# Kernel optimization log

Measured on AMD Instinct MI355X. Metric: run time of the kernel, lower is better.

The kernel has to match this reference:

```python
import jax, jax.numpy as jnp
import numpy as np

B, S, N, E = 8, 32, 2000, 64000
GH, H = 32, 64  # gat_h, lstm hidden
NEG_SLOPE = 0.2


def setup_inputs() -> dict:
    key = jax.random.key(0)
    ks = jax.random.split(key, 12)
    f32 = jnp.float32
    x = jax.random.normal(ks[0], (B, S, N), f32)
    edge_index = jax.random.randint(ks[1], (2, E), 0, N)
    # GATConv(1, GH, heads=1, concat=False): lin weight [GH,1] -> vector, att_src/att_dst [GH], bias [GH]
    w_lin = jax.random.normal(ks[2], (GH,), f32)
    att_src = jax.random.normal(ks[3], (GH,), f32) * 0.1
    att_dst = jax.random.normal(ks[4], (GH,), f32) * 0.1
    gat_bias = jax.random.normal(ks[5], (GH,), f32) * 0.01
    D = GH * N  # LSTM input size
    W_ih = jax.random.normal(ks[6], (4 * H, D), f32) * (1.0 / np.sqrt(D))
    W_hh = jax.random.normal(ks[7], (4 * H, H), f32) * (1.0 / np.sqrt(H))
    b_ih = jax.random.normal(ks[8], (4 * H,), f32) * 0.01
    b_hh = jax.random.normal(ks[9], (4 * H,), f32) * 0.01
    W_head = jax.random.normal(ks[10], (N, H), f32) * (1.0 / np.sqrt(H))
    b_head = jax.random.normal(ks[11], (N,), f32) * 0.01
    return {"x": x, "edge_index": edge_index, "w_lin": w_lin, "att_src": att_src,
            "att_dst": att_dst, "gat_bias": gat_bias, "W_ih": W_ih, "W_hh": W_hh,
            "b_ih": b_ih, "b_hh": b_hh, "W_head": W_head, "b_head": b_head}


def reference(x, edge_index, w_lin, att_src, att_dst, gat_bias,
              W_ih, W_hh, b_ih, b_hh, W_head, b_head):
    x = x.astype(jnp.float32)
    # --- GAT (in_channels=1, heads=1), batched over (B,S) ---
    # PyG default: add self-loops
    loops = jnp.arange(N)
    ei = jnp.concatenate([edge_index, jnp.stack([loops, loops])], axis=1)
    src, dst = ei[0], ei[1]  # [Et], Et = E + N
    # lifted feature h_n = x_n * w_lin (rank-1), so attention logits are scalar per node
    a_src = x * jnp.dot(w_lin, att_src)  # [B,S,N]
    a_dst = x * jnp.dot(w_lin, att_dst)  # [B,S,N]
    e = jax.nn.leaky_relu(a_src[..., src] + a_dst[..., dst], NEG_SLOPE)  # [B,S,Et]
    e = jnp.moveaxis(e, -1, 0)  # [Et,B,S] (segment axis leading)
    seg_max = jax.ops.segment_max(e, dst, num_segments=N)  # [N,B,S]
    e = jnp.exp(e - seg_max[dst])
    denom = jax.ops.segment_sum(e, dst, num_segments=N)  # [N,B,S]
    alpha = e / denom[dst]  # edge softmax over incoming edges
    x_src = jnp.moveaxis(x[..., src], -1, 0)  # [Et,B,S]
    agg = jax.ops.segment_sum(alpha * x_src, dst, num_segments=N)  # [N,B,S]
    agg = jnp.moveaxis(agg, 0, -1)  # [B,S,N]
    # outer product with w_lin restores [.,GH]; add bias, then relu (from forward)
    h = jax.nn.relu(agg[..., None] * w_lin + gat_bias)  # [B,S,N,GH]
    lstm_in = h.reshape(B, S, N * GH)

    # --- LSTM (1 layer, batch_first), keep final hidden state ---
    def step(carry, xt):
        hp, cp = carry
        gates = xt @ W_ih.T + b_ih + hp @ W_hh.T + b_hh  # [B,4H]
        i, f, g, o = jnp.split(gates, 4, axis=-1)
        c = jax.nn.sigmoid(f) * cp + jax.nn.sigmoid(i) * jnp.tanh(g)
        hn = jax.nn.sigmoid(o) * jnp.tanh(c)
        return (hn, c), None

    h0 = jnp.zeros((B, H), jnp.float32)
    c0 = jnp.zeros((B, H), jnp.float32)
    (hT, _), _ = jax.lax.scan(step, (h0, c0), jnp.swapaxes(lstm_in, 0, 1))
    return hT @ W_head.T + b_head  # [B,N]
```

## Files before the change

### kernel.cpp

```cpp
#include <hip/hip_runtime.h>
#include <hip/hip_bf16.h>
#include <cstddef>
#include <cstdint>

#define B_  8
#define S_  32
#define BT_ 256
#define N_  2000
#define E_  64000
#define GH_ 32
#define H_  64
#define G4_ 256
#define D_  64000
#define NEG_SLOPE_ 0.2f

#define KC_   125
#define NPC_  16

typedef __attribute__((ext_vector_type(8))) short short8;
typedef __attribute__((ext_vector_type(4))) float floatx4;
union U8 { uint32_t u[4]; short8 s; };

__device__ __forceinline__ float fsigmoid(float x) { return 1.0f / (1.0f + __expf(-x)); }
__device__ __forceinline__ float ftanh_(float x)   { return 1.0f - 2.0f / (__expf(2.0f * x) + 1.0f); }

__device__ __forceinline__ void split2(float v0, float v1, uint32_t& hi, uint32_t& lo) {
  uint32_t b0 = __float_as_uint(v0), b1 = __float_as_uint(v1);
  uint32_t h0 = b0 & 0xffff0000u,    h1 = b1 & 0xffff0000u;
  hi = (b0 >> 16) | h1;
  float l0 = v0 - __uint_as_float(h0);
  float l1 = v1 - __uint_as_float(h1);
  lo = (__float_as_uint(l0) >> 16) | (__float_as_uint(l1) & 0xffff0000u);
}


__global__ __launch_bounds__(256) void hist_kernel(
    const int* __restrict__ ei, int* __restrict__ deg)
{
  const int i = blockIdx.x * 256 + threadIdx.x;
  if (i < E_) atomicAdd(&deg[ei[E_ + i]], 1);
}

__global__ __launch_bounds__(256) void scan_kernel(
    const int* __restrict__ deg, int* __restrict__ rowptr, int* __restrict__ cursor)
{
  __shared__ int tsum[256];
  const int tid = threadIdx.x;
  int v[8];
  int s = 0;
  const int base = tid * 8;
#pragma unroll
  for (int j = 0; j < 8; ++j) {
    const int idx = base + j;
    const int d = (idx < N_) ? deg[idx] : 0;
    v[j] = s;
    s += d;
  }
  tsum[tid] = s;
  __syncthreads();
  for (int off = 1; off < 256; off <<= 1) {
    int t = 0;
    if (tid >= off) t = tsum[tid - off];
    __syncthreads();
    tsum[tid] += t;
    __syncthreads();
  }
  const int ebase = tsum[tid] - s;
#pragma unroll
  for (int j = 0; j < 8; ++j) {
    const int idx = base + j;
    if (idx < N_) {
      const int r = ebase + v[j];
      rowptr[idx] = r;
      cursor[idx] = r;
    }
  }
  if (tid == 0) rowptr[N_] = E_;
}

__global__ __launch_bounds__(256) void scatter_kernel(
    const int* __restrict__ ei, int* __restrict__ cursor, int* __restrict__ csr_src)
{
  const int i = blockIdx.x * 256 + threadIdx.x;
  if (i >= E_) return;
  const int s = ei[i];
  const int d = ei[E_ + i];
  const int pos = atomicAdd(&cursor[d], 1);
  csr_src[pos] = s;
}

__global__ __launch_bounds__(256) void transpose_kernel(
    const float* __restrict__ x, float* __restrict__ xT)
{
  __shared__ float tile[32][33];
  const int tx = threadIdx.x & 31;
  const int ty = threadIdx.x >> 5;
  const int n0  = blockIdx.x * 32;
  const int bt0 = blockIdx.y * 32;
#pragma unroll
  for (int r = 0; r < 4; ++r) {
    const int bt = bt0 + ty + r * 8;
    const int nn = n0 + tx;
    if (nn < N_) tile[ty + r * 8][tx] = x[(size_t)bt * N_ + nn];
  }
  __syncthreads();
#pragma unroll
  for (int r = 0; r < 4; ++r) {
    const int n = n0 + ty + r * 8;
    if (n < N_) xT[(size_t)n * BT_ + bt0 + tx] = tile[tx][ty + r * 8];
  }
}

__global__ __launch_bounds__(256) void gat_gather_kernel(
    const float* __restrict__ xT, const int* __restrict__ rowptr,
    const int* __restrict__ csr_src,
    const float* __restrict__ w_lin, const float* __restrict__ att_src,
    const float* __restrict__ att_dst, float* __restrict__ agg_T)
{
  __shared__ int srcs[512];
  const int n   = blockIdx.x;
  const int tid = threadIdx.x;

  float c_s = 0.f, c_d = 0.f;
  for (int g = 0; g < GH_; ++g) {
    const float w = w_lin[g];
    c_s += w * att_src[g];
    c_d += w * att_dst[g];
  }

  const int r0 = rowptr[n];
  const int r1 = rowptr[n + 1];
  const int d  = r1 - r0;
  for (int i = tid; i < d && i < 512; i += 256) srcs[i] = csr_src[r0 + i];
  __syncthreads();

  const float xn = xT[(size_t)n * BT_ + tid];
  float e = (c_s + c_d) * xn;
  e = e > 0.f ? e : NEG_SLOPE_ * e;
  float w = __expf(e);
  float num = w * xn;
  float den = w;

  for (int p = 0; p < d; ++p) {
    int s;
    if (p < 512) s = srcs[p]; else s = csr_src[r0 + p];
    const float xs = xT[(size_t)s * BT_ + tid];
    float ee = c_s * xs + c_d * xn;
    ee = ee > 0.f ? ee : NEG_SLOPE_ * ee;
    const float ww = __expf(ee);
    num += ww * xs;
    den += ww;
  }
  agg_T[(size_t)n * BT_ + tid] = num / den;
}

__global__ __launch_bounds__(256) void gate_mfma_kernel(
    const float* __restrict__ W_ih, const float* __restrict__ agg_T,
    const float* __restrict__ w_lin, const float* __restrict__ gat_bias,
    float* __restrict__ partial, float* __restrict__ pre_gates, int use_atomic)
{
  __shared__ float agg_s[NPC_ * 256];

  const int tid  = threadIdx.x;
  const int nb   = blockIdx.x;
  const int kc   = blockIdx.y;
  const int n0   = kc * NPC_;
  const int wv   = tid >> 6;
  const int lane = tid & 63;
  const int i16  = lane & 15;
  const int q    = lane >> 4;
  const int jw   = nb * 64 + wv * 16;

  {
    const float4* src = (const float4*)(agg_T + (size_t)n0 * 256);
    float4* dst = (float4*)agg_s;
#pragma unroll
    for (int p = 0; p < 4; ++p) dst[tid + p * 256] = src[tid + p * 256];
  }

  float wlr[8], gbr[8];
#pragma unroll
  for (int j = 0; j < 8; ++j) {
    wlr[j] = w_lin[q * 8 + j];
    gbr[j] = gat_bias[q * 8 + j];
  }

  floatx4 acc[16];
#pragma unroll
  for (int mt = 0; mt < 16; ++mt)
#pragma unroll
    for (int r = 0; r < 4; ++r) acc[mt][r] = 0.f;

  __syncthreads();

  const float* Wrow = W_ih + (size_t)(jw + i16) * D_ + (size_t)n0 * GH_ + q * 8;

  float4 cb0 = *(const float4*)(Wrow);
  float4 cb1 = *(const float4*)(Wrow + 4);

#pragma unroll 1
  for (int nn = 0; nn < NPC_; ++nn) {
    const int nnx = (nn + 1) & (NPC_ - 1);
    float4 pb0 = *(const float4*)(Wrow + nnx * GH_);
    float4 pb1 = *(const float4*)(Wrow + nnx * GH_ + 4);

    short8 bh, bl;
    {
      U8 Hh, Ll;
      split2(cb0.x, cb0.y, Hh.u[0], Ll.u[0]);
      split2(cb0.z, cb0.w, Hh.u[1], Ll.u[1]);
      split2(cb1.x, cb1.y, Hh.u[2], Ll.u[2]);
      split2(cb1.z, cb1.w, Hh.u[3], Ll.u[3]);
      bh = Hh.s; bl = Ll.s;
    }

#pragma unroll
    for (int mt = 0; mt < 16; ++mt) {
      const float a = agg_s[nn * 256 + mt * 16 + i16];
      U8 Ah, Al;
#pragma unroll
      for (int p = 0; p < 4; ++p) {
        float v0 = fmaf(a, wlr[2 * p],     gbr[2 * p]);
        float v1 = fmaf(a, wlr[2 * p + 1], gbr[2 * p + 1]);
        v0 = fmaxf(v0, 0.f);
        v1 = fmaxf(v1, 0.f);
        split2(v0, v1, Ah.u[p], Al.u[p]);
      }
      acc[mt] = __builtin_amdgcn_mfma_f32_16x16x32_bf16(Ah.s, bh, acc[mt], 0, 0, 0);
      acc[mt] = __builtin_amdgcn_mfma_f32_16x16x32_bf16(Al.s, bh, acc[mt], 0, 0, 0);
      acc[mt] = __builtin_amdgcn_mfma_f32_16x16x32_bf16(Ah.s, bl, acc[mt], 0, 0, 0);
    }
    cb0 = pb0; cb1 = pb1;
  }

  const int j = jw + i16;
#pragma unroll
  for (int mt = 0; mt < 16; ++mt) {
    const int bt = mt * 16 + q * 4;
    if (use_atomic) {
#pragma unroll
      for (int r = 0; r < 4; ++r) atomicAdd(&pre_gates[(bt + r) * G4_ + j], acc[mt][r]);
    } else {
#pragma unroll
      for (int r = 0; r < 4; ++r)
        partial[((size_t)kc * 256 + (bt + r)) * 256 + j] = acc[mt][r];
    }
  }
}

__global__ __launch_bounds__(256) void reduce_kernel(
    const float* __restrict__ partial, float* __restrict__ pre_gates)
{
  const int o = blockIdx.x * 256 + threadIdx.x;
  float s0 = 0.f, s1 = 0.f, s2 = 0.f, s3 = 0.f;
  int kc = 0;
  for (; kc + 4 <= KC_; kc += 4) {
    s0 += partial[(size_t)(kc + 0) * 65536 + o];
    s1 += partial[(size_t)(kc + 1) * 65536 + o];
    s2 += partial[(size_t)(kc + 2) * 65536 + o];
    s3 += partial[(size_t)(kc + 3) * 65536 + o];
  }
  for (; kc < KC_; ++kc) s0 += partial[(size_t)kc * 65536 + o];
  pre_gates[o] = (s0 + s1) + (s2 + s3);
}

__global__ __launch_bounds__(256) void lstm_kernel(
    const float* __restrict__ pre_gates, const float* __restrict__ W_hh,
    const float* __restrict__ b_ih, const float* __restrict__ b_hh,
    float* __restrict__ hT)
{
  const int b   = blockIdx.x;
  const int tid = threadIdx.x;
  __shared__ float h_s[H_];
  __shared__ float g_s[G4_];

  float wr[H_];
#pragma unroll
  for (int k = 0; k < H_; ++k) wr[k] = W_hh[(size_t)tid * H_ + k];

  float pg[S_];
#pragma unroll
  for (int t = 0; t < S_; ++t) pg[t] = pre_gates[(size_t)(b * S_ + t) * G4_ + tid];

  const float bias = b_ih[tid] + b_hh[tid];
  if (tid < H_) h_s[tid] = 0.f;
  float c = 0.f;
  __syncthreads();

  for (int t = 0; t < S_; ++t) {
    float g0 = pg[t] + bias, g1 = 0.f, g2 = 0.f, g3 = 0.f;
#pragma unroll
    for (int k = 0; k < H_; k += 4) {
      g0 = fmaf(wr[k + 0], h_s[k + 0], g0);
      g1 = fmaf(wr[k + 1], h_s[k + 1], g1);
      g2 = fmaf(wr[k + 2], h_s[k + 2], g2);
      g3 = fmaf(wr[k + 3], h_s[k + 3], g3);
    }
    g_s[tid] = (g0 + g1) + (g2 + g3);
    __syncthreads();
    if (tid < H_) {
      const float ig = fsigmoid(g_s[tid]);
      const float fg = fsigmoid(g_s[H_ + tid]);
      const float gg = ftanh_(g_s[2 * H_ + tid]);
      const float og = fsigmoid(g_s[3 * H_ + tid]);
      c = fg * c + ig * gg;
      h_s[tid] = og * ftanh_(c);
    }
    __syncthreads();
  }
  if (tid < H_) hT[b * H_ + tid] = h_s[tid];
}

__global__ __launch_bounds__(256) void head_kernel(
    const float* __restrict__ hT, const float* __restrict__ W_head,
    const float* __restrict__ b_head, float* __restrict__ out)
{
  const int o = blockIdx.x * 256 + threadIdx.x;
  if (o >= B_ * N_) return;
  const int b = o / N_;
  const int n = o - b * N_;
  const float4* w4 = (const float4*)(W_head + (size_t)n * H_);
  const float4* h4 = (const float4*)(hT + (size_t)b * H_);
  float acc = b_head[n];
#pragma unroll
  for (int q = 0; q < H_ / 4; ++q) {
    const float4 w = w4[q];
    const float4 h = h4[q];
    acc += w.x * h.x + w.y * h.y + w.z * h.z + w.w * h.w;
  }
  out[o] = acc;
}

extern "C" void kernel_launch(void* const* d_in, const int* in_sizes, int n_in,
                              void* d_out, int out_size, void* d_ws, size_t ws_size,
                              hipStream_t stream) {
  const float* x        = (const float*)d_in[0];
  const int*   ei       = (const int*)  d_in[1];
  const float* w_lin    = (const float*)d_in[2];
  const float* att_src  = (const float*)d_in[3];
  const float* att_dst  = (const float*)d_in[4];
  const float* gat_bias = (const float*)d_in[5];
  const float* W_ih     = (const float*)d_in[6];
  const float* W_hh     = (const float*)d_in[7];
  const float* b_ih     = (const float*)d_in[8];
  const float* b_hh     = (const float*)d_in[9];
  const float* W_head   = (const float*)d_in[10];
  const float* b_head   = (const float*)d_in[11];
  float* out = (float*)d_out;

  char* ws = (char*)d_ws;
  float* agg_T     = (float*)(ws + 0);
  float* pre_gates = (float*)(ws + 2048000);
  float* hT        = (float*)(ws + 2310144);
  float* xT        = (float*)(ws + 2312192);
  int*   deg       = (int*)  (ws + 4360192);
  int*   rowptr    = (int*)  (ws + 4368384);
  int*   cursor    = (int*)  (ws + 4376576);
  int*   csr_src   = (int*)  (ws + 4384768);
  float* partial   = (float*)(ws + 4640768);
  const size_t need = 4640768 + (size_t)KC_ * 65536 * sizeof(float);
  const int use_atomic = (ws_size < need) ? 1 : 0;

  hipMemsetAsync(deg, 0, N_ * sizeof(int), stream);
  hist_kernel<<<dim3((E_ + 255) / 256), dim3(256), 0, stream>>>(ei, deg);
  scan_kernel<<<dim3(1), dim3(256), 0, stream>>>(deg, rowptr, cursor);
  scatter_kernel<<<dim3((E_ + 255) / 256), dim3(256), 0, stream>>>(ei, cursor, csr_src);
  transpose_kernel<<<dim3((N_ + 31) / 32, BT_ / 32), dim3(256), 0, stream>>>(x, xT);
  gat_gather_kernel<<<dim3(N_), dim3(256), 0, stream>>>(
      xT, rowptr, csr_src, w_lin, att_src, att_dst, agg_T);

  if (use_atomic) {
    hipMemsetAsync(pre_gates, 0, G4_ * BT_ * sizeof(float), stream);
  }
  gate_mfma_kernel<<<dim3(4, KC_), dim3(256), 0, stream>>>(
      W_ih, agg_T, w_lin, gat_bias, partial, pre_gates, use_atomic);
  if (!use_atomic) {
    reduce_kernel<<<dim3(256), dim3(256), 0, stream>>>(partial, pre_gates);
  }

  lstm_kernel<<<dim3(B_), dim3(256), 0, stream>>>(pre_gates, W_hh, b_ih, b_hh, hT);
  head_kernel<<<dim3((B_ * N_ + 255) / 256), dim3(256), 0, stream>>>(hT, W_head, b_head, out);
}
```

Measured before the change: 249.4 us.

## Materialize fp16 GAT features and switch gate GEMM to single fp16 MFMA

The GAT gather kernel now expands each aggregated value through w_lin, bias and ReLU and writes a 32-wide fp16 feature tensor (about 32 MB). The gate GEMM reads this directly and uses one fp16 MFMA per tile instead of three bf16 split-precision MFMAs, with a new tiling of 8x50 blocks, 40 nodes per chunk and fewer partials to reduce. CSR construction is merged into a single-block kernel using shared-memory atomics, and the head projection is fused into the LSTM kernel. This drops precision to plain fp16 and adds a large extra memory write and read in exchange for fewer MFMAs and fewer launches.

```diff
diff --git a/kernel.cpp b/kernel.cpp
--- a/kernel.cpp
+++ b/kernel.cpp
@@ -14,79 +14,54 @@
 #define D_  64000
 #define NEG_SLOPE_ 0.2f
 
-#define KC_   125
-#define NPC_  16
-
-typedef __attribute__((ext_vector_type(8))) short short8;
+#define KC2_  50
+#define NPC2_ 40
+
+typedef __attribute__((ext_vector_type(8))) _Float16 half8;
 typedef __attribute__((ext_vector_type(4))) float floatx4;
-union U8 { uint32_t u[4]; short8 s; };
 
 __device__ __forceinline__ float fsigmoid(float x) { return 1.0f / (1.0f + __expf(-x)); }
 __device__ __forceinline__ float ftanh_(float x)   { return 1.0f - 2.0f / (__expf(2.0f * x) + 1.0f); }
 
-__device__ __forceinline__ void split2(float v0, float v1, uint32_t& hi, uint32_t& lo) {
-  uint32_t b0 = __float_as_uint(v0), b1 = __float_as_uint(v1);
-  uint32_t h0 = b0 & 0xffff0000u,    h1 = b1 & 0xffff0000u;
-  hi = (b0 >> 16) | h1;
-  float l0 = v0 - __uint_as_float(h0);
-  float l1 = v1 - __uint_as_float(h1);
-  lo = (__float_as_uint(l0) >> 16) | (__float_as_uint(l1) & 0xffff0000u);
-}
-
-
-__global__ __launch_bounds__(256) void hist_kernel(
-    const int* __restrict__ ei, int* __restrict__ deg)
-{
-  const int i = blockIdx.x * 256 + threadIdx.x;
-  if (i < E_) atomicAdd(&deg[ei[E_ + i]], 1);
-}
-
-__global__ __launch_bounds__(256) void scan_kernel(
-    const int* __restrict__ deg, int* __restrict__ rowptr, int* __restrict__ cursor)
-{
-  __shared__ int tsum[256];
+__global__ __launch_bounds__(1024) void csr_build_kernel(
+    const int* __restrict__ ei, int* __restrict__ rowptr, int* __restrict__ csr_src)
+{
+  __shared__ int deg_s[N_];
+  __shared__ int cur_s[N_];
+  __shared__ int tsum[1024];
   const int tid = threadIdx.x;
-  int v[8];
-  int s = 0;
-  const int base = tid * 8;
-#pragma unroll
-  for (int j = 0; j < 8; ++j) {
-    const int idx = base + j;
-    const int d = (idx < N_) ? deg[idx] : 0;
-    v[j] = s;
-    s += d;
-  }
-  tsum[tid] = s;
-  __syncthreads();
-  for (int off = 1; off < 256; off <<= 1) {
+
+  for (int n = tid; n < N_; n += 1024) deg_s[n] = 0;
+  __syncthreads();
+
+  for (int i = tid; i < E_; i += 1024) atomicAdd(&deg_s[ei[E_ + i]], 1);
+  __syncthreads();
+
+  const int i0 = tid * 2, i1 = tid * 2 + 1;
+  const int d0 = (i0 < N_) ? deg_s[i0] : 0;
+  const int d1 = (i1 < N_) ? deg_s[i1] : 0;
+  const int sl = d0 + d1;
+  tsum[tid] = sl;
+  __syncthreads();
+  for (int off = 1; off < 1024; off <<= 1) {
     int t = 0;
     if (tid >= off) t = tsum[tid - off];
     __syncthreads();
     tsum[tid] += t;
     __syncthreads();
   }
-  const int ebase = tsum[tid] - s;
-#pragma unroll
-  for (int j = 0; j < 8; ++j) {
-    const int idx = base + j;
-    if (idx < N_) {
-      const int r = ebase + v[j];
-      rowptr[idx] = r;
-      cursor[idx] = r;
-    }
-  }
+  const int ebase = tsum[tid] - sl;
+  if (i0 < N_) { rowptr[i0] = ebase;      cur_s[i0] = ebase; }
+  if (i1 < N_) { rowptr[i1] = ebase + d0; cur_s[i1] = ebase + d0; }
   if (tid == 0) rowptr[N_] = E_;
-}
-
-__global__ __launch_bounds__(256) void scatter_kernel(
-    const int* __restrict__ ei, int* __restrict__ cursor, int* __restrict__ csr_src)
-{
-  const int i = blockIdx.x * 256 + threadIdx.x;
-  if (i >= E_) return;
-  const int s = ei[i];
-  const int d = ei[E_ + i];
-  const int pos = atomicAdd(&cursor[d], 1);
-  csr_src[pos] = s;
+  __syncthreads();
+
+  for (int i = tid; i < E_; i += 1024) {
+    const int s = ei[i];
+    const int d = ei[E_ + i];
+    const int pos = atomicAdd(&cur_s[d], 1);
+    csr_src[pos] = s;
+  }
 }
 
 __global__ __launch_bounds__(256) void transpose_kernel(
@@ -111,13 +86,15 @@
   }
 }
 
-__global__ __launch_bounds__(256) void gat_gather_kernel(
+__global__ __launch_bounds__(256) void gat_gather_expand_kernel(
     const float* __restrict__ xT, const int* __restrict__ rowptr,
     const int* __restrict__ csr_src,
     const float* __restrict__ w_lin, const float* __restrict__ att_src,
-    const float* __restrict__ att_dst, float* __restrict__ agg_T)
+    const float* __restrict__ att_dst, const float* __restrict__ gat_bias,
+    _Float16* __restrict__ A)
 {
   __shared__ int srcs[512];
+  __shared__ float wl_s[GH_], gb_s[GH_];
   const int n   = blockIdx.x;
   const int tid = threadIdx.x;
 
@@ -127,6 +104,7 @@
     c_s += w * att_src[g];
     c_d += w * att_dst[g];
   }
+  if (tid < GH_) { wl_s[tid] = w_lin[tid]; gb_s[tid] = gat_bias[tid]; }
 
   const int r0 = rowptr[n];
   const int r1 = rowptr[n + 1];
@@ -151,99 +129,105 @@
     num += ww * xs;
     den += ww;
   }
-  agg_T[(size_t)n * BT_ + tid] = num / den;
-}
-
-__global__ __launch_bounds__(256) void gate_mfma_kernel(
-    const float* __restrict__ W_ih, const float* __restrict__ agg_T,
-    const float* __restrict__ w_lin, const float* __restrict__ gat_bias,
+  const float aggv = num / den;
+
+  half8 buf[4];
+#pragma unroll
+  for (int q = 0; q < 4; ++q)
+#pragma unroll
+    for (int j = 0; j < 8; ++j) {
+      const int g = q * 8 + j;
+      float v = fmaf(aggv, wl_s[g], gb_s[g]);
+      v = fmaxf(v, 0.f);
+      buf[q][j] = (_Float16)v;
+    }
+  half8* dst = (half8*)(A + ((size_t)n * BT_ + tid) * GH_);
+#pragma unroll
+  for (int q = 0; q < 4; ++q) dst[q] = buf[q];
+}
+
+__global__ __launch_bounds__(256) void gate_mfma2_kernel(
+    const float* __restrict__ W_ih, const _Float16* __restrict__ A,
     float* __restrict__ partial, float* __restrict__ pre_gates, int use_atomic)
 {
-  __shared__ float agg_s[NPC_ * 256];
-
   const int tid  = threadIdx.x;
   const int nb   = blockIdx.x;
   const int kc   = blockIdx.y;
-  const int n0   = kc * NPC_;
+  const int n0   = kc * NPC2_;
   const int wv   = tid >> 6;
   const int lane = tid & 63;
   const int i16  = lane & 15;
   const int q    = lane >> 4;
-  const int jw   = nb * 64 + wv * 16;
-
-  {
-    const float4* src = (const float4*)(agg_T + (size_t)n0 * 256);
-    float4* dst = (float4*)agg_s;
-#pragma unroll
-    for (int p = 0; p < 4; ++p) dst[tid + p * 256] = src[tid + p * 256];
-  }
-
-  float wlr[8], gbr[8];
-#pragma unroll
-  for (int j = 0; j < 8; ++j) {
-    wlr[j] = w_lin[q * 8 + j];
-    gbr[j] = gat_bias[q * 8 + j];
-  }
-
-  floatx4 acc[16];
-#pragma unroll
-  for (int mt = 0; mt < 16; ++mt)
-#pragma unroll
-    for (int r = 0; r < 4; ++r) acc[mt][r] = 0.f;
-
-  __syncthreads();
-
-  const float* Wrow = W_ih + (size_t)(jw + i16) * D_ + (size_t)n0 * GH_ + q * 8;
-
-  float4 cb0 = *(const float4*)(Wrow);
-  float4 cb1 = *(const float4*)(Wrow + 4);
+  const int jn0  = nb * 32;
+
+  floatx4 acc[4][2];
+#pragma unroll
+  for (int mt = 0; mt < 4; ++mt)
+#pragma unroll
+    for (int nt = 0; nt < 2; ++nt)
+#pragma unroll
+      for (int r = 0; r < 4; ++r) acc[mt][nt][r] = 0.f;
+
+  const _Float16* Ap = A + ((size_t)n0 * BT_ + wv * 64 + i16) * GH_ + q * 8;
+
+  const float* Bp0 = W_ih + (size_t)(jn0 + i16) * D_ + (size_t)n0 * GH_ + q * 8;
+  const float* Bp1 = Bp0 + (size_t)16 * D_;
+
+  float4 b0a = *(const float4*)(Bp0);
+  float4 b0b = *(const float4*)(Bp0 + 4);
+  float4 b1a = *(const float4*)(Bp1);
+  float4 b1b = *(const float4*)(Bp1 + 4);
 
 #pragma unroll 1
-  for (int nn = 0; nn < NPC_; ++nn) {
-    const int nnx = (nn + 1) & (NPC_ - 1);
-    float4 pb0 = *(const float4*)(Wrow + nnx * GH_);
-    float4 pb1 = *(const float4*)(Wrow + nnx * GH_ + 4);
-
-    short8 bh, bl;
-    {
-      U8 Hh, Ll;
-      split2(cb0.x, cb0.y, Hh.u[0], Ll.u[0]);
-      split2(cb0.z, cb0.w, Hh.u[1], Ll.u[1]);
-      split2(cb1.x, cb1.y, Hh.u[2], Ll.u[2]);
-      split2(cb1.z, cb1.w, Hh.u[3], Ll.u[3]);
-      bh = Hh.s; bl = Ll.s;
-    }
-
-#pragma unroll
-    for (int mt = 0; mt < 16; ++mt) {
-      const float a = agg_s[nn * 256 + mt * 16 + i16];
-      U8 Ah, Al;
-#pragma unroll
-      for (int p = 0; p < 4; ++p) {
-        float v0 = fmaf(a, wlr[2 * p],     gbr[2 * p]);
-        float v1 = fmaf(a, wlr[2 * p + 1], gbr[2 * p + 1]);
-        v0 = fmaxf(v0, 0.f);
-        v1 = fmaxf(v1, 0.f);
-        split2(v0, v1, Ah.u[p], Al.u[p]);
+  for (int nn = 0; nn < NPC2_; ++nn) {
+    half8 a0 = *(const half8*)(Ap + 0 * 512);
+    half8 a1 = *(const half8*)(Ap + 1 * 512);
+    half8 a2 = *(const half8*)(Ap + 2 * 512);
+    half8 a3 = *(const half8*)(Ap + 3 * 512);
+
+    const int nx = (nn + 1 < NPC2_) ? (nn + 1) : nn;
+    float4 p0a = *(const float4*)(Bp0 + nx * GH_);
+    float4 p0b = *(const float4*)(Bp0 + nx * GH_ + 4);
+    float4 p1a = *(const float4*)(Bp1 + nx * GH_);
+    float4 p1b = *(const float4*)(Bp1 + nx * GH_ + 4);
+
+    half8 bf0, bf1;
+    bf0[0] = (_Float16)b0a.x; bf0[1] = (_Float16)b0a.y;
+    bf0[2] = (_Float16)b0a.z; bf0[3] = (_Float16)b0a.w;
+    bf0[4] = (_Float16)b0b.x; bf0[5] = (_Float16)b0b.y;
+    bf0[6] = (_Float16)b0b.z; bf0[7] = (_Float16)b0b.w;
+    bf1[0] = (_Float16)b1a.x; bf1[1] = (_Float16)b1a.y;
+    bf1[2] = (_Float16)b1a.z; bf1[3] = (_Float16)b1a.w;
+    bf1[4] = (_Float16)b1b.x; bf1[5] = (_Float16)b1b.y;
+    bf1[6] = (_Float16)b1b.z; bf1[7] = (_Float16)b1b.w;
+
+    acc[0][0] = __builtin_amdgcn_mfma_f32_16x16x32_f16(a0, bf0, acc[0][0], 0, 0, 0);
+    acc[1][0] = __builtin_amdgcn_mfma_f32_16x16x32_f16(a1, bf0, acc[1][0], 0, 0, 0);
+    acc[2][0] = __builtin_amdgcn_mfma_f32_16x16x32_f16(a2, bf0, acc[2][0], 0, 0, 0);
+    acc[3][0] = __builtin_amdgcn_mfma_f32_16x16x32_f16(a3, bf0, acc[3][0], 0, 0, 0);
+    acc[0][1] = __builtin_amdgcn_mfma_f32_16x16x32_f16(a0, bf1, acc[0][1], 0, 0, 0);
+    acc[1][1] = __builtin_amdgcn_mfma_f32_16x16x32_f16(a1, bf1, acc[1][1], 0, 0, 0);
+    acc[2][1] = __builtin_amdgcn_mfma_f32_16x16x32_f16(a2, bf1, acc[2][1], 0, 0, 0);
+    acc[3][1] = __builtin_amdgcn_mfma_f32_16x16x32_f16(a3, bf1, acc[3][1], 0, 0, 0);
+
+    b0a = p0a; b0b = p0b; b1a = p1a; b1b = p1b;
+    Ap += (size_t)BT_ * GH_;
+  }
+
+#pragma unroll
+  for (int mt = 0; mt < 4; ++mt) {
+    const int bt = wv * 64 + mt * 16 + q * 4;
+#pragma unroll
+    for (int nt = 0; nt < 2; ++nt) {
+      const int j = jn0 + nt * 16 + i16;
+      if (use_atomic) {
+#pragma unroll
+        for (int r = 0; r < 4; ++r) atomicAdd(&pre_gates[(bt + r) * G4_ + j], acc[mt][nt][r]);
+      } else {
+#pragma unroll
+        for (int r = 0; r < 4; ++r)
+          partial[((size_t)kc * BT_ + (bt + r)) * G4_ + j] = acc[mt][nt][r];
       }
-      acc[mt] = __builtin_amdgcn_mfma_f32_16x16x32_bf16(Ah.s, bh, acc[mt], 0, 0, 0);
-      acc[mt] = __builtin_amdgcn_mfma_f32_16x16x32_bf16(Al.s, bh, acc[mt], 0, 0, 0);
-      acc[mt] = __builtin_amdgcn_mfma_f32_16x16x32_bf16(Ah.s, bl, acc[mt], 0, 0, 0);
-    }
-    cb0 = pb0; cb1 = pb1;
-  }
-
-  const int j = jw + i16;
-#pragma unroll
-  for (int mt = 0; mt < 16; ++mt) {
-    const int bt = mt * 16 + q * 4;
-    if (use_atomic) {
-#pragma unroll
-      for (int r = 0; r < 4; ++r) atomicAdd(&pre_gates[(bt + r) * G4_ + j], acc[mt][r]);
-    } else {
-#pragma unroll
-      for (int r = 0; r < 4; ++r)
-        partial[((size_t)kc * 256 + (bt + r)) * 256 + j] = acc[mt][r];
     }
   }
 }
@@ -252,22 +236,21 @@
     const float* __restrict__ partial, float* __restrict__ pre_gates)
 {
   const int o = blockIdx.x * 256 + threadIdx.x;
-  float s0 = 0.f, s1 = 0.f, s2 = 0.f, s3 = 0.f;
+  float s0 = 0.f, s1 = 0.f;
   int kc = 0;
-  for (; kc + 4 <= KC_; kc += 4) {
+  for (; kc + 2 <= KC2_; kc += 2) {
     s0 += partial[(size_t)(kc + 0) * 65536 + o];
     s1 += partial[(size_t)(kc + 1) * 65536 + o];
-    s2 += partial[(size_t)(kc + 2) * 65536 + o];
-    s3 += partial[(size_t)(kc + 3) * 65536 + o];
-  }
-  for (; kc < KC_; ++kc) s0 += partial[(size_t)kc * 65536 + o];
-  pre_gates[o] = (s0 + s1) + (s2 + s3);
-}
-
-__global__ __launch_bounds__(256) void lstm_kernel(
+  }
+  for (; kc < KC2_; ++kc) s0 += partial[(size_t)kc * 65536 + o];
+  pre_gates[o] = s0 + s1;
+}
+
+__global__ __launch_bounds__(256) void lstm_head_kernel(
     const float* __restrict__ pre_gates, const float* __restrict__ W_hh,
     const float* __restrict__ b_ih, const float* __restrict__ b_hh,
-    float* __restrict__ hT)
+    const float* __restrict__ W_head, const float* __restrict__ b_head,
+    float* __restrict__ out)
 {
   const int b   = blockIdx.x;
   const int tid = threadIdx.x;
@@ -308,27 +291,18 @@
     }
     __syncthreads();
   }
-  if (tid < H_) hT[b * H_ + tid] = h_s[tid];
-}
-
-__global__ __launch_bounds__(256) void head_kernel(
-    const float* __restrict__ hT, const float* __restrict__ W_head,
-    const float* __restrict__ b_head, float* __restrict__ out)
-{
-  const int o = blockIdx.x * 256 + threadIdx.x;
-  if (o >= B_ * N_) return;
-  const int b = o / N_;
-  const int n = o - b * N_;
-  const float4* w4 = (const float4*)(W_head + (size_t)n * H_);
-  const float4* h4 = (const float4*)(hT + (size_t)b * H_);
-  float acc = b_head[n];
-#pragma unroll
-  for (int q = 0; q < H_ / 4; ++q) {
-    const float4 w = w4[q];
-    const float4 h = h4[q];
-    acc += w.x * h.x + w.y * h.y + w.z * h.z + w.w * h.w;
-  }
-  out[o] = acc;
+
+  for (int n = tid; n < N_; n += 256) {
+    const float4* w4 = (const float4*)(W_head + (size_t)n * H_);
+    float acc = b_head[n];
+#pragma unroll
+    for (int qq = 0; qq < H_ / 4; ++qq) {
+      const float4 w = w4[qq];
+      acc += w.x * h_s[qq * 4 + 0] + w.y * h_s[qq * 4 + 1] +
+             w.z * h_s[qq * 4 + 2] + w.w * h_s[qq * 4 + 3];
+    }
+    out[(size_t)b * N_ + n] = acc;
+  }
 }
 
 extern "C" void kernel_launch(void* const* d_in, const int* in_sizes, int n_in,
@@ -349,35 +323,29 @@
   float* out = (float*)d_out;
 
   char* ws = (char*)d_ws;
-  float* agg_T     = (float*)(ws + 0);
-  float* pre_gates = (float*)(ws + 2048000);
-  float* hT        = (float*)(ws + 2310144);
-  float* xT        = (float*)(ws + 2312192);
-  int*   deg       = (int*)  (ws + 4360192);
-  int*   rowptr    = (int*)  (ws + 4368384);
-  int*   cursor    = (int*)  (ws + 4376576);
-  int*   csr_src   = (int*)  (ws + 4384768);
-  float* partial   = (float*)(ws + 4640768);
-  const size_t need = 4640768 + (size_t)KC_ * 65536 * sizeof(float);
+  float*     xT        = (float*)    (ws + 0);
+  _Float16*  A         = (_Float16*) (ws + 2048000);
+  float*     pre_gates = (float*)    (ws + 34816000);
+  int*       rowptr    = (int*)      (ws + 35078144);
+  int*       csr_src   = (int*)      (ws + 35086336);
+  float*     partial   = (float*)    (ws + 35342336);
+  const size_t need = 35342336 + (size_t)KC2_ * 65536 * sizeof(float);
   const int use_atomic = (ws_size < need) ? 1 : 0;
 
-  hipMemsetAsync(deg, 0, N_ * sizeof(int), stream);
-  hist_kernel<<<dim3((E_ + 255) / 256), dim3(256), 0, stream>>>(ei, deg);
-  scan_kernel<<<dim3(1), dim3(256), 0, stream>>>(deg, rowptr, cursor);
-  scatter_kernel<<<dim3((E_ + 255) / 256), dim3(256), 0, stream>>>(ei, cursor, csr_src);
+  csr_build_kernel<<<dim3(1), dim3(1024), 0, stream>>>(ei, rowptr, csr_src);
   transpose_kernel<<<dim3((N_ + 31) / 32, BT_ / 32), dim3(256), 0, stream>>>(x, xT);
-  gat_gather_kernel<<<dim3(N_), dim3(256), 0, stream>>>(
-      xT, rowptr, csr_src, w_lin, att_src, att_dst, agg_T);
+  gat_gather_expand_kernel<<<dim3(N_), dim3(256), 0, stream>>>(
+      xT, rowptr, csr_src, w_lin, att_src, att_dst, gat_bias, A);
 
   if (use_atomic) {
     hipMemsetAsync(pre_gates, 0, G4_ * BT_ * sizeof(float), stream);
   }
-  gate_mfma_kernel<<<dim3(4, KC_), dim3(256), 0, stream>>>(
-      W_ih, agg_T, w_lin, gat_bias, partial, pre_gates, use_atomic);
+  gate_mfma2_kernel<<<dim3(8, KC2_), dim3(256), 0, stream>>>(
+      W_ih, A, partial, pre_gates, use_atomic);
   if (!use_atomic) {
     reduce_kernel<<<dim3(256), dim3(256), 0, stream>>>(partial, pre_gates);
   }
 
-  lstm_kernel<<<dim3(B_), dim3(256), 0, stream>>>(pre_gates, W_hh, b_ih, b_hh, hT);
-  head_kernel<<<dim3((B_ * N_ + 255) / 256), dim3(256), 0, stream>>>(hT, W_head, b_head, out);
-}
+  lstm_head_kernel<<<dim3(B_), dim3(256), 0, stream>>>(
+      pre_gates, W_hh, b_ih, b_hh, W_head, b_head, out);
+}
```

Measured after the change: 312.1 us. +25.1%, slower.

## Switch gate GEMM to single fp16 MFMA and fuse prep and head kernels

Applied to the files above, without the earlier changes.

The W_ih gate GEMM now converts both operands to fp16 and issues one MFMA per tile, replacing the three-pass bf16 hi/lo split emulation of fp32. It is retiled to 8x64 blocks with per-wave 4x2 tiles, and agg is read directly from global memory instead of being staged through shared memory. The degree memset is folded into the transpose kernel, the head projection is fused into the LSTM kernel, the atomic fallback path is removed, and the gather loop is unrolled by four. Dropping the split passes cuts MFMA and conversion work by about a factor of three, at the cost of fp16 rounding on a reduction of length 64000.

```diff
diff --git a/kernel.cpp b/kernel.cpp
--- a/kernel.cpp
+++ b/kernel.cpp
@@ -13,35 +13,50 @@
 #define G4_ 256
 #define D_  64000
 #define NEG_SLOPE_ 0.2f
-
-#define KC_   125
-#define NPC_  16
-
-typedef __attribute__((ext_vector_type(8))) short short8;
+#define KC_  64
+
+typedef __attribute__((ext_vector_type(8))) _Float16 half8;
 typedef __attribute__((ext_vector_type(4))) float floatx4;
-union U8 { uint32_t u[4]; short8 s; };
 
 __device__ __forceinline__ float fsigmoid(float x) { return 1.0f / (1.0f + __expf(-x)); }
 __device__ __forceinline__ float ftanh_(float x)   { return 1.0f - 2.0f / (__expf(2.0f * x) + 1.0f); }
 
-__device__ __forceinline__ void split2(float v0, float v1, uint32_t& hi, uint32_t& lo) {
-  uint32_t b0 = __float_as_uint(v0), b1 = __float_as_uint(v1);
-  uint32_t h0 = b0 & 0xffff0000u,    h1 = b1 & 0xffff0000u;
-  hi = (b0 >> 16) | h1;
-  float l0 = v0 - __uint_as_float(h0);
-  float l1 = v1 - __uint_as_float(h1);
-  lo = (__float_as_uint(l0) >> 16) | (__float_as_uint(l1) & 0xffff0000u);
-}
-
-
-__global__ __launch_bounds__(256) void hist_kernel(
+__global__ __launch_bounds__(256) void k_prep(
+    const float* __restrict__ x, float* __restrict__ xT, int* __restrict__ deg)
+{
+  const int gt = blockIdx.x * 256 + threadIdx.x;
+  if (gt < N_) deg[gt] = 0;
+
+  __shared__ float tile[32][33];
+  const int TXT = (N_ + 31) / 32;
+  const int t = blockIdx.x;
+  if (t >= TXT * (BT_ / 32)) return;
+  const int tx = threadIdx.x & 31;
+  const int ty = threadIdx.x >> 5;
+  const int n0  = (t % TXT) * 32;
+  const int bt0 = (t / TXT) * 32;
+#pragma unroll
+  for (int r = 0; r < 4; ++r) {
+    const int bt = bt0 + ty + r * 8;
+    const int nn = n0 + tx;
+    if (nn < N_) tile[ty + r * 8][tx] = x[(size_t)bt * N_ + nn];
+  }
+  __syncthreads();
+#pragma unroll
+  for (int r = 0; r < 4; ++r) {
+    const int n = n0 + ty + r * 8;
+    if (n < N_) xT[(size_t)n * BT_ + bt0 + tx] = tile[tx][ty + r * 8];
+  }
+}
+
+__global__ __launch_bounds__(256) void k_hist(
     const int* __restrict__ ei, int* __restrict__ deg)
 {
   const int i = blockIdx.x * 256 + threadIdx.x;
   if (i < E_) atomicAdd(&deg[ei[E_ + i]], 1);
 }
 
-__global__ __launch_bounds__(256) void scan_kernel(
+__global__ __launch_bounds__(256) void k_scan(
     const int* __restrict__ deg, int* __restrict__ rowptr, int* __restrict__ cursor)
 {
   __shared__ int tsum[256];
@@ -78,7 +93,7 @@
   if (tid == 0) rowptr[N_] = E_;
 }
 
-__global__ __launch_bounds__(256) void scatter_kernel(
+__global__ __launch_bounds__(256) void k_scatter(
     const int* __restrict__ ei, int* __restrict__ cursor, int* __restrict__ csr_src)
 {
   const int i = blockIdx.x * 256 + threadIdx.x;
@@ -89,185 +104,166 @@
   csr_src[pos] = s;
 }
 
-__global__ __launch_bounds__(256) void transpose_kernel(
-    const float* __restrict__ x, float* __restrict__ xT)
-{
-  __shared__ float tile[32][33];
-  const int tx = threadIdx.x & 31;
-  const int ty = threadIdx.x >> 5;
-  const int n0  = blockIdx.x * 32;
-  const int bt0 = blockIdx.y * 32;
-#pragma unroll
-  for (int r = 0; r < 4; ++r) {
-    const int bt = bt0 + ty + r * 8;
-    const int nn = n0 + tx;
-    if (nn < N_) tile[ty + r * 8][tx] = x[(size_t)bt * N_ + nn];
-  }
-  __syncthreads();
-#pragma unroll
-  for (int r = 0; r < 4; ++r) {
-    const int n = n0 + ty + r * 8;
-    if (n < N_) xT[(size_t)n * BT_ + bt0 + tx] = tile[tx][ty + r * 8];
-  }
-}
-
-__global__ __launch_bounds__(256) void gat_gather_kernel(
+__global__ __launch_bounds__(256) void k_gather(
     const float* __restrict__ xT, const int* __restrict__ rowptr,
     const int* __restrict__ csr_src,
     const float* __restrict__ w_lin, const float* __restrict__ att_src,
-    const float* __restrict__ att_dst, float* __restrict__ agg_T)
-{
-  __shared__ int srcs[512];
+    const float* __restrict__ att_dst, float* __restrict__ agg)
+{
   const int n   = blockIdx.x;
   const int tid = threadIdx.x;
-
   float c_s = 0.f, c_d = 0.f;
   for (int g = 0; g < GH_; ++g) {
     const float w = w_lin[g];
     c_s += w * att_src[g];
     c_d += w * att_dst[g];
   }
-
   const int r0 = rowptr[n];
-  const int r1 = rowptr[n + 1];
-  const int d  = r1 - r0;
-  for (int i = tid; i < d && i < 512; i += 256) srcs[i] = csr_src[r0 + i];
-  __syncthreads();
-
+  const int d  = rowptr[n + 1] - r0;
   const float xn = xT[(size_t)n * BT_ + tid];
+  const float cdxn = c_d * xn;
   float e = (c_s + c_d) * xn;
   e = e > 0.f ? e : NEG_SLOPE_ * e;
-  float w = __expf(e);
-  float num = w * xn;
-  float den = w;
-
-  for (int p = 0; p < d; ++p) {
-    int s;
-    if (p < 512) s = srcs[p]; else s = csr_src[r0 + p];
+  const float w0 = __expf(e);
+  float num = w0 * xn, den = w0;
+  int pp = 0;
+  for (; pp + 4 <= d; pp += 4) {
+    const int s0 = csr_src[r0 + pp + 0];
+    const int s1 = csr_src[r0 + pp + 1];
+    const int s2 = csr_src[r0 + pp + 2];
+    const int s3 = csr_src[r0 + pp + 3];
+    const float x0 = xT[(size_t)s0 * BT_ + tid];
+    const float x1 = xT[(size_t)s1 * BT_ + tid];
+    const float x2 = xT[(size_t)s2 * BT_ + tid];
+    const float x3 = xT[(size_t)s3 * BT_ + tid];
+    float e0 = fmaf(c_s, x0, cdxn); e0 = e0 > 0.f ? e0 : NEG_SLOPE_ * e0;
+    float e1 = fmaf(c_s, x1, cdxn); e1 = e1 > 0.f ? e1 : NEG_SLOPE_ * e1;
+    float e2 = fmaf(c_s, x2, cdxn); e2 = e2 > 0.f ? e2 : NEG_SLOPE_ * e2;
+    float e3 = fmaf(c_s, x3, cdxn); e3 = e3 > 0.f ? e3 : NEG_SLOPE_ * e3;
+    const float w0_ = __expf(e0), w1_ = __expf(e1), w2_ = __expf(e2), w3_ = __expf(e3);
+    num += w0_ * x0 + w1_ * x1 + w2_ * x2 + w3_ * x3;
+    den += (w0_ + w1_) + (w2_ + w3_);
+  }
+  for (; pp < d; ++pp) {
+    const int s = csr_src[r0 + pp];
     const float xs = xT[(size_t)s * BT_ + tid];
-    float ee = c_s * xs + c_d * xn;
+    float ee = fmaf(c_s, xs, cdxn);
     ee = ee > 0.f ? ee : NEG_SLOPE_ * ee;
     const float ww = __expf(ee);
     num += ww * xs;
     den += ww;
   }
-  agg_T[(size_t)n * BT_ + tid] = num / den;
-}
-
-__global__ __launch_bounds__(256) void gate_mfma_kernel(
-    const float* __restrict__ W_ih, const float* __restrict__ agg_T,
+  agg[(size_t)n * BT_ + tid] = num / den;
+}
+
+__global__ __launch_bounds__(256) void k_mfma(
+    const float* __restrict__ W_ih, const float* __restrict__ agg,
     const float* __restrict__ w_lin, const float* __restrict__ gat_bias,
-    float* __restrict__ partial, float* __restrict__ pre_gates, int use_atomic)
-{
-  __shared__ float agg_s[NPC_ * 256];
-
+    float* __restrict__ partial)
+{
+  const int nb = blockIdx.x;
+  const int kc = blockIdx.y;
+  const int n0 = (N_ * kc) / KC_;
+  const int n1 = (N_ * (kc + 1)) / KC_;
   const int tid  = threadIdx.x;
-  const int nb   = blockIdx.x;
-  const int kc   = blockIdx.y;
-  const int n0   = kc * NPC_;
   const int wv   = tid >> 6;
   const int lane = tid & 63;
   const int i16  = lane & 15;
   const int q    = lane >> 4;
-  const int jw   = nb * 64 + wv * 16;
-
-  {
-    const float4* src = (const float4*)(agg_T + (size_t)n0 * 256);
-    float4* dst = (float4*)agg_s;
-#pragma unroll
-    for (int p = 0; p < 4; ++p) dst[tid + p * 256] = src[tid + p * 256];
-  }
-
-  float wlr[8], gbr[8];
+  const int j0   = nb * 32;
+
+  float wlq[8], gbq[8];
 #pragma unroll
   for (int j = 0; j < 8; ++j) {
-    wlr[j] = w_lin[q * 8 + j];
-    gbr[j] = gat_bias[q * 8 + j];
-  }
-
-  floatx4 acc[16];
-#pragma unroll
-  for (int mt = 0; mt < 16; ++mt)
-#pragma unroll
-    for (int r = 0; r < 4; ++r) acc[mt][r] = 0.f;
-
-  __syncthreads();
-
-  const float* Wrow = W_ih + (size_t)(jw + i16) * D_ + (size_t)n0 * GH_ + q * 8;
-
-  float4 cb0 = *(const float4*)(Wrow);
-  float4 cb1 = *(const float4*)(Wrow + 4);
+    wlq[j] = w_lin[q * 8 + j];
+    gbq[j] = gat_bias[q * 8 + j];
+  }
+
+  floatx4 acc[4][2];
+#pragma unroll
+  for (int mt = 0; mt < 4; ++mt)
+#pragma unroll
+    for (int nt = 0; nt < 2; ++nt)
+#pragma unroll
+      for (int r = 0; r < 4; ++r) acc[mt][nt][r] = 0.f;
+
+  const float* Bp0 = W_ih + (size_t)(j0 + i16) * D_ + (size_t)n0 * GH_ + q * 8;
+  const float* Bp1 = Bp0 + (size_t)16 * D_;
+
+  float4 c0a = *(const float4*)(Bp0);
+  float4 c0b = *(const float4*)(Bp0 + 4);
+  float4 c1a = *(const float4*)(Bp1);
+  float4 c1b = *(const float4*)(Bp1 + 4);
 
 #pragma unroll 1
-  for (int nn = 0; nn < NPC_; ++nn) {
-    const int nnx = (nn + 1) & (NPC_ - 1);
-    float4 pb0 = *(const float4*)(Wrow + nnx * GH_);
-    float4 pb1 = *(const float4*)(Wrow + nnx * GH_ + 4);
-
-    short8 bh, bl;
-    {
-      U8 Hh, Ll;
-      split2(cb0.x, cb0.y, Hh.u[0], Ll.u[0]);
-      split2(cb0.z, cb0.w, Hh.u[1], Ll.u[1]);
-      split2(cb1.x, cb1.y, Hh.u[2], Ll.u[2]);
-      split2(cb1.z, cb1.w, Hh.u[3], Ll.u[3]);
-      bh = Hh.s; bl = Ll.s;
-    }
-
-#pragma unroll
-    for (int mt = 0; mt < 16; ++mt) {
-      const float a = agg_s[nn * 256 + mt * 16 + i16];
-      U8 Ah, Al;
-#pragma unroll
-      for (int p = 0; p < 4; ++p) {
-        float v0 = fmaf(a, wlr[2 * p],     gbr[2 * p]);
-        float v1 = fmaf(a, wlr[2 * p + 1], gbr[2 * p + 1]);
-        v0 = fmaxf(v0, 0.f);
-        v1 = fmaxf(v1, 0.f);
-        split2(v0, v1, Ah.u[p], Al.u[p]);
+  for (int nn = n0; nn < n1; ++nn) {
+    const int nx = (nn + 1 < n1) ? (nn + 1 - n0) : (nn - n0);
+    const int off = nx * GH_;
+    float4 p0a = *(const float4*)(Bp0 + off);
+    float4 p0b = *(const float4*)(Bp0 + off + 4);
+    float4 p1a = *(const float4*)(Bp1 + off);
+    float4 p1b = *(const float4*)(Bp1 + off + 4);
+
+    half8 bf0, bf1;
+    bf0[0] = (_Float16)c0a.x; bf0[1] = (_Float16)c0a.y;
+    bf0[2] = (_Float16)c0a.z; bf0[3] = (_Float16)c0a.w;
+    bf0[4] = (_Float16)c0b.x; bf0[5] = (_Float16)c0b.y;
+    bf0[6] = (_Float16)c0b.z; bf0[7] = (_Float16)c0b.w;
+    bf1[0] = (_Float16)c1a.x; bf1[1] = (_Float16)c1a.y;
+    bf1[2] = (_Float16)c1a.z; bf1[3] = (_Float16)c1a.w;
+    bf1[4] = (_Float16)c1b.x; bf1[5] = (_Float16)c1b.y;
+    bf1[6] = (_Float16)c1b.z; bf1[7] = (_Float16)c1b.w;
+
+    const float* Ar = agg + (size_t)nn * BT_ + wv * 64 + i16;
+#pragma unroll
+    for (int mt = 0; mt < 4; ++mt) {
+      const float a = Ar[mt * 16];
+      half8 af;
+#pragma unroll
+      for (int j = 0; j < 8; ++j) {
+        float v = fmaf(a, wlq[j], gbq[j]);
+        v = fmaxf(v, 0.f);
+        af[j] = (_Float16)v;
       }
-      acc[mt] = __builtin_amdgcn_mfma_f32_16x16x32_bf16(Ah.s, bh, acc[mt], 0, 0, 0);
-      acc[mt] = __builtin_amdgcn_mfma_f32_16x16x32_bf16(Al.s, bh, acc[mt], 0, 0, 0);
-      acc[mt] = __builtin_amdgcn_mfma_f32_16x16x32_bf16(Ah.s, bl, acc[mt], 0, 0, 0);
-    }
-    cb0 = pb0; cb1 = pb1;
-  }
-
-  const int j = jw + i16;
-#pragma unroll
-  for (int mt = 0; mt < 16; ++mt) {
-    const int bt = mt * 16 + q * 4;
-    if (use_atomic) {
-#pragma unroll
-      for (int r = 0; r < 4; ++r) atomicAdd(&pre_gates[(bt + r) * G4_ + j], acc[mt][r]);
-    } else {
+      acc[mt][0] = __builtin_amdgcn_mfma_f32_16x16x32_f16(af, bf0, acc[mt][0], 0, 0, 0);
+      acc[mt][1] = __builtin_amdgcn_mfma_f32_16x16x32_f16(af, bf1, acc[mt][1], 0, 0, 0);
+    }
+    c0a = p0a; c0b = p0b; c1a = p1a; c1b = p1b;
+  }
+
+#pragma unroll
+  for (int mt = 0; mt < 4; ++mt) {
+    const int bt = wv * 64 + mt * 16 + q * 4;
+#pragma unroll
+    for (int nt = 0; nt < 2; ++nt) {
+      const int j = j0 + nt * 16 + i16;
 #pragma unroll
       for (int r = 0; r < 4; ++r)
-        partial[((size_t)kc * 256 + (bt + r)) * 256 + j] = acc[mt][r];
-    }
-  }
-}
-
-__global__ __launch_bounds__(256) void reduce_kernel(
+        partial[(size_t)kc * 65536 + (size_t)(bt + r) * G4_ + j] = acc[mt][nt][r];
+    }
+  }
+}
+
+__global__ __launch_bounds__(256) void k_reduce(
     const float* __restrict__ partial, float* __restrict__ pre_gates)
 {
   const int o = blockIdx.x * 256 + threadIdx.x;
   float s0 = 0.f, s1 = 0.f, s2 = 0.f, s3 = 0.f;
-  int kc = 0;
-  for (; kc + 4 <= KC_; kc += 4) {
+#pragma unroll
+  for (int kc = 0; kc < KC_; kc += 4) {
     s0 += partial[(size_t)(kc + 0) * 65536 + o];
     s1 += partial[(size_t)(kc + 1) * 65536 + o];
     s2 += partial[(size_t)(kc + 2) * 65536 + o];
     s3 += partial[(size_t)(kc + 3) * 65536 + o];
   }
-  for (; kc < KC_; ++kc) s0 += partial[(size_t)kc * 65536 + o];
   pre_gates[o] = (s0 + s1) + (s2 + s3);
 }
 
-__global__ __launch_bounds__(256) void lstm_kernel(
+__global__ __launch_bounds__(256) void k_lstm_head(
     const float* __restrict__ pre_gates, const float* __restrict__ W_hh,
     const float* __restrict__ b_ih, const float* __restrict__ b_hh,
-    float* __restrict__ hT)
+    const float* __restrict__ W_head, const float* __restrict__ b_head,
+    float* __restrict__ out)
 {
   const int b   = blockIdx.x;
   const int tid = threadIdx.x;
@@ -277,7 +273,6 @@
   float wr[H_];
 #pragma unroll
   for (int k = 0; k < H_; ++k) wr[k] = W_hh[(size_t)tid * H_ + k];
-
   float pg[S_];
 #pragma unroll
   for (int t = 0; t < S_; ++t) pg[t] = pre_gates[(size_t)(b * S_ + t) * G4_ + tid];
@@ -308,27 +303,18 @@
     }
     __syncthreads();
   }
-  if (tid < H_) hT[b * H_ + tid] = h_s[tid];
-}
-
-__global__ __launch_bounds__(256) void head_kernel(
-    const float* __restrict__ hT, const float* __restrict__ W_head,
-    const float* __restrict__ b_head, float* __restrict__ out)
-{
-  const int o = blockIdx.x * 256 + threadIdx.x;
-  if (o >= B_ * N_) return;
-  const int b = o / N_;
-  const int n = o - b * N_;
-  const float4* w4 = (const float4*)(W_head + (size_t)n * H_);
-  const float4* h4 = (const float4*)(hT + (size_t)b * H_);
-  float acc = b_head[n];
-#pragma unroll
-  for (int q = 0; q < H_ / 4; ++q) {
-    const float4 w = w4[q];
-    const float4 h = h4[q];
-    acc += w.x * h.x + w.y * h.y + w.z * h.z + w.w * h.w;
-  }
-  out[o] = acc;
+
+  for (int n = tid; n < N_; n += 256) {
+    const float4* w4 = (const float4*)(W_head + (size_t)n * H_);
+    float acc = b_head[n];
+#pragma unroll
+    for (int qq = 0; qq < H_ / 4; ++qq) {
+      const float4 w = w4[qq];
+      acc += w.x * h_s[qq * 4 + 0] + w.y * h_s[qq * 4 + 1] +
+             w.z * h_s[qq * 4 + 2] + w.w * h_s[qq * 4 + 3];
+    }
+    out[(size_t)b * N_ + n] = acc;
+  }
 }
 
 extern "C" void kernel_launch(void* const* d_in, const int* in_sizes, int n_in,
@@ -349,35 +335,24 @@
   float* out = (float*)d_out;
 
   char* ws = (char*)d_ws;
-  float* agg_T     = (float*)(ws + 0);
-  float* pre_gates = (float*)(ws + 2048000);
-  float* hT        = (float*)(ws + 2310144);
-  float* xT        = (float*)(ws + 2312192);
-  int*   deg       = (int*)  (ws + 4360192);
-  int*   rowptr    = (int*)  (ws + 4368384);
-  int*   cursor    = (int*)  (ws + 4376576);
-  int*   csr_src   = (int*)  (ws + 4384768);
-  float* partial   = (float*)(ws + 4640768);
-  const size_t need = 4640768 + (size_t)KC_ * 65536 * sizeof(float);
-  const int use_atomic = (ws_size < need) ? 1 : 0;
-
-  hipMemsetAsync(deg, 0, N_ * sizeof(int), stream);
-  hist_kernel<<<dim3((E_ + 255) / 256), dim3(256), 0, stream>>>(ei, deg);
-  scan_kernel<<<dim3(1), dim3(256), 0, stream>>>(deg, rowptr, cursor);
-  scatter_kernel<<<dim3((E_ + 255) / 256), dim3(256), 0, stream>>>(ei, cursor, csr_src);
-  transpose_kernel<<<dim3((N_ + 31) / 32, BT_ / 32), dim3(256), 0, stream>>>(x, xT);
-  gat_gather_kernel<<<dim3(N_), dim3(256), 0, stream>>>(
-      xT, rowptr, csr_src, w_lin, att_src, att_dst, agg_T);
-
-  if (use_atomic) {
-    hipMemsetAsync(pre_gates, 0, G4_ * BT_ * sizeof(float), stream);
-  }
-  gate_mfma_kernel<<<dim3(4, KC_), dim3(256), 0, stream>>>(
-      W_ih, agg_T, w_lin, gat_bias, partial, pre_gates, use_atomic);
-  if (!use_atomic) {
-    reduce_kernel<<<dim3(256), dim3(256), 0, stream>>>(partial, pre_gates);
-  }
-
-  lstm_kernel<<<dim3(B_), dim3(256), 0, stream>>>(pre_gates, W_hh, b_ih, b_hh, hT);
-  head_kernel<<<dim3((B_ * N_ + 255) / 256), dim3(256), 0, stream>>>(hT, W_head, b_head, out);
-}
+  float* xT        = (float*)(ws + 0);
+  float* agg       = (float*)(ws + 2048000);
+  float* pre_gates = (float*)(ws + 4096000);
+  int*   deg       = (int*)  (ws + 4358144);
+  int*   rowptr    = (int*)  (ws + 4366336);
+  int*   cursor    = (int*)  (ws + 4374528);
+  int*   csr_src   = (int*)  (ws + 4382720);
+  float* partial   = (float*)(ws + 4638720);
+
+  k_prep<<<dim3(504), dim3(256), 0, stream>>>(x, xT, deg);
+  k_hist<<<dim3((E_ + 255) / 256), dim3(256), 0, stream>>>(ei, deg);
+  k_scan<<<dim3(1), dim3(256), 0, stream>>>(deg, rowptr, cursor);
+  k_scatter<<<dim3((E_ + 255) / 256), dim3(256), 0, stream>>>(ei, cursor, csr_src);
+  k_gather<<<dim3(N_), dim3(256), 0, stream>>>(
+      xT, rowptr, csr_src, w_lin, att_src, att_dst, agg);
+  k_mfma<<<dim3(8, KC_), dim3(256), 0, stream>>>(
+      W_ih, agg, w_lin, gat_bias, partial);
+  k_reduce<<<dim3(256), dim3(256), 0, stream>>>(partial, pre_gates);
+  k_lstm_head<<<dim3(B_), dim3(256), 0, stream>>>(
+      pre_gates, W_hh, b_ih, b_hh, W_head, b_head, out);
+}
```

Result: slower. 261.5 us (+4.8%).
